# Optimization experiments

Measured on AMD Instinct MI355X. Metric: run time of the kernel, lower is better.

The kernel has to match this reference:

```python
import math
import jax, jax.numpy as jnp
import numpy as np

IN_CH = 64
NUM_ANCHOR = 4
MAP_H, MAP_W = 96, 96
BATCH = 8
BN_EPS = 1e-5


def _conv2d(x, w, b, padding, dilation):
    # x: [B,C,H,W], w: [O,I,kh,kw] (OIHW)
    y = jax.lax.conv_general_dilated(
        x, w, window_strides=(1, 1),
        padding=((padding, padding), (padding, padding)),
        rhs_dilation=(dilation, dilation),
        dimension_numbers=('NCHW', 'OIHW', 'NCHW'))
    return y + b[None, :, None, None]


def _bn(x, gamma, beta, mean, var):
    scale = gamma / jnp.sqrt(var + BN_EPS)
    return x * scale[None, :, None, None] + (beta - mean * scale)[None, :, None, None]


def setup_inputs() -> dict:
    key = jax.random.key(0)
    ks = jax.random.split(key, 12)
    # cyclic channel-shift permutation matrices, one per anchor pass
    eye = np.eye(IN_CH, dtype=np.float32)
    shift = IN_CH // (2 * NUM_ANCHOR)
    perms = np.stack([eye[np.roll(np.arange(IN_CH), i * shift)] for i in range(2 * NUM_ANCHOR)])
    w_std = 1.0 / math.sqrt(IN_CH * 9)
    return {
        'x': jax.random.normal(ks[0], (BATCH, IN_CH, MAP_H, MAP_W), dtype=jnp.float32),
        'perms': jnp.asarray(perms),
        'dcn_w': jax.random.normal(ks[1], (IN_CH, IN_CH, 3, 3), dtype=jnp.float32) * w_std,
        'dcn_b': jax.random.normal(ks[2], (IN_CH,), dtype=jnp.float32) * 0.01,
        'conv2_w': jax.random.normal(ks[3], (IN_CH, IN_CH, 3, 3), dtype=jnp.float32) * w_std,
        'conv2_b': jax.random.normal(ks[4], (IN_CH,), dtype=jnp.float32) * 0.01,
        'conv3_w': jax.random.normal(ks[5], (IN_CH, IN_CH, 3, 3), dtype=jnp.float32) * w_std,
        'conv3_b': jax.random.normal(ks[6], (IN_CH,), dtype=jnp.float32) * 0.01,
        'bn_gamma': jax.random.uniform(ks[7], (3, IN_CH), dtype=jnp.float32, minval=0.5, maxval=1.5),
        'bn_beta': jax.random.normal(ks[8], (3, IN_CH), dtype=jnp.float32) * 0.1,
        'bn_mean': jax.random.normal(ks[9], (3, IN_CH), dtype=jnp.float32) * 0.1,
        'bn_var': jax.random.uniform(ks[10], (3, IN_CH), dtype=jnp.float32, minval=0.5, maxval=1.5),
    }


def reference(x, perms, dcn_w, dcn_b, conv2_w, conv2_b, conv3_w, conv3_b,
              bn_gamma, bn_beta, bn_mean, bn_var):
    h = x.shape[2]
    pad = math.ceil(h / (2 ** 1.5 + 2))  # 20 for h=96

    def conv_stack(o):
        # DCN at init (zero offsets) == plain 3x3 conv, pad=1
        o = jax.nn.relu(_bn(_conv2d(o, dcn_w, dcn_b, 1, 1), bn_gamma[0], bn_beta[0], bn_mean[0], bn_var[0]))
        o = jax.nn.relu(_bn(_conv2d(o, conv2_w, conv2_b, 2, 2), bn_gamma[1], bn_beta[1], bn_mean[1], bn_var[1]))
        o = jax.nn.relu(_bn(_conv2d(o, conv3_w, conv3_b, 2, 2), bn_gamma[2], bn_beta[2], bn_mean[2], bn_var[2]))
        return o

    outs = []
    for i in range(2 * NUM_ANCHOR):  # fixed small structural loop
        o = jnp.einsum('mn,bnhw->bmhw', perms[i], x)  # channel permutation
        if i % 2 != 0:
            o = jnp.pad(o, ((0, 0), (0, 0), (pad, pad), (pad, pad)))
        o = jnp.rot90(o, k=i % 4, axes=(-2, -1))   # ccw rotate
        o = conv_stack(o)
        o = jnp.rot90(o, k=(-i) % 4, axes=(-2, -1))  # cw rotate back
        if i % 2 != 0:
            H, W = o.shape[-2], o.shape[-1]
            sh, sw = (H - MAP_H) // 2, (W - MAP_W) // 2
            o = o[..., sh:sh + MAP_H, sw:sw + MAP_W]  # center crop
        outs.append(o)
    out_tensor = jnp.concatenate(outs, axis=1)  # [B, 8*C, H, W]
    out = jnp.max(out_tensor, axis=1, keepdims=True)
    # branch_name == 'midpoint', orientational_anchor=False -> clamped sigmoid
    return jnp.clip(jax.nn.sigmoid(out), 1e-4, 1.0 - 1e-4)
```

## Files before the change

### kernel.cpp

```cpp
#include <hip/hip_runtime.h>
#include <math.h>

#define B 8
#define C 64
#define HW 96
#define NWV 36864

typedef __attribute__((ext_vector_type(8)))  short short8;
typedef __attribute__((ext_vector_type(16))) float floatx16;

__device__ __forceinline__ unsigned short f2bf(float f) {
    unsigned int u = __float_as_uint(f);
    unsigned int r = (u + 0x7fffu + ((u >> 16) & 1u)) >> 16;
    return (unsigned short)r;
}

__device__ __forceinline__ void rotmap(int k, int ta, int tb, int& sa, int& sb) {
    switch (k) {
        case 0: sa = ta;     sb = tb;     break;
        case 1: sa = 2 - tb; sb = ta;     break;
        case 2: sa = 2 - ta; sb = 2 - tb; break;
        default: sa = tb;    sb = 2 - ta; break;
    }
}

__global__ void prep_w(const float* __restrict__ dcn_w, const float* __restrict__ c2w,
                       const float* __restrict__ c3w,
                       const float* __restrict__ gamma, const float* __restrict__ var_,
                       unsigned short* __restrict__ Wall) {
    int idx = blockIdx.x * 256 + threadIdx.x;
    if (idx >= 16 * NWV) return;
    int v = idx / NWV, rem = idx % NWV;
    int tap  = rem >> 12;
    int w12  = rem & 4095;
    int ks   = w12 >> 10;
    int cf   = (w12 >> 9) & 1;
    int lane = (w12 >> 3) & 63;
    int j    = w12 & 7;
    int co = cf * 32 + (lane & 31);
    int ci = ks * 16 + (lane >> 5) * 8 + j;
    int ta = tap / 3, tb = tap % 3;
    const float* src; int k, srcci, l;
    if (v < 8)       { k = v & 3;  srcci = (ci + 8 * v) & 63; src = dcn_w; l = 0; }
    else if (v < 12) { k = v - 8;  srcci = ci; src = c2w; l = 1; }
    else             { k = v - 12; srcci = ci; src = c3w; l = 2; }
    int sa, sb; rotmap(k, ta, tb, sa, sb);
    float s = gamma[l * 64 + co] * rsqrtf(var_[l * 64 + co] + 1e-5f);
    Wall[idx] = f2bf(src[((co * 64 + srcci) * 3 + sa) * 3 + sb] * s);
}

__global__ void prep_bias(const float* __restrict__ dcn_b, const float* __restrict__ c2b,
                          const float* __restrict__ c3b,
                          const float* __restrict__ gamma, const float* __restrict__ beta,
                          const float* __restrict__ mean, const float* __restrict__ var_,
                          float* __restrict__ biasg) {
    int t = threadIdx.x;
    if (t < 192) {
        int l = t >> 6, c = t & 63;
        const float* cb = (l == 0) ? dcn_b : ((l == 1) ? c2b : c3b);
        float s = gamma[l * 64 + c] * rsqrtf(var_[l * 64 + c] + 1e-5f);
        biasg[t] = cb[c] * s + beta[l * 64 + c] - mean[l * 64 + c] * s;
    }
}

__global__ __launch_bounds__(256) void prep_x(const float* __restrict__ in,
                                              unsigned short* __restrict__ out) {
    __shared__ float row[64 * 97];
    int by = blockIdx.x;
    int b = by / 96, y = by % 96;
    int t = threadIdx.x;
    for (int e = t; e < 6144; e += 256) {
        int c = e / 96, x = e - c * 96;
        row[c * 97 + x] = in[(((size_t)(b * 64 + c) * 96 + y) * 96) + x];
    }
    __syncthreads();
    for (int e = t; e < 6144; e += 256) {
        int x = e >> 6, c = e & 63;
        out[(((size_t)(b * 96 + y) * 96 + x) << 6) + c] = f2bf(row[c * 97 + x]);
    }
}

__global__ __launch_bounds__(256) void border_clear(unsigned short* __restrict__ buf1) {
    int idx = blockIdx.y;
    int br = (idx >> 3) * 2, b = idx & 7;
    int z = br * 8 + b;
    int i = blockIdx.x * 32 + (threadIdx.x >> 3);
    int g = threadIdx.x & 7;
    int r, c;
    if (i < 416)      { r = i / 104;              c = i % 104; }
    else if (i < 832) { int j = i - 416; r = 100 + j / 104; c = j % 104; }
    else              { int j = i - 832; r = 4 + (j >> 3); int c8 = j & 7;
                        c = (c8 < 4) ? c8 : 92 + c8; }
    uint4 zero = make_uint4(0u, 0u, 0u, 0u);
    *(uint4*)(buf1 + (size_t)z * (104 * 104 * 64) + ((size_t)(r * 104 + c) << 6) + (g << 3)) = zero;
}

__global__ __launch_bounds__(256, 2) void conv1_k(
    const unsigned short* __restrict__ xhwc, unsigned short* __restrict__ buf1,
    const unsigned short* __restrict__ Wall, const float* __restrict__ biasg) {

    __shared__ __align__(16) unsigned short xt[10 * 34 * 64];

    int z = blockIdx.z, br = z >> 3, b = z & 7, odd = br & 1;
    int fy0 = blockIdx.y * 8, fx0 = blockIdx.x * 32;
    int t = threadIdx.x, lane = t & 63, wv = t >> 6;
    int n = lane & 31, kq = lane >> 5;

    const unsigned short* xb = xhwc + ((size_t)b * 96 * 96 << 6);
    const short8* Ag = (const short8*)(Wall + (size_t)br * NWV);

    for (int e = t; e < 2720; e += 256) {
        int p = e >> 3, g = e & 7;
        int yy = p / 34, xx = p - yy * 34;
        int gy = fy0 - 5 + yy, gx = fx0 - 5 + xx;
        uint4 v = make_uint4(0u, 0u, 0u, 0u);
        if ((unsigned)gy < 96u && (unsigned)gx < 96u)
            v = *(const uint4*)(xb + ((size_t)(gy * 96 + gx) << 6) + (g << 3));
        *(uint4*)(xt + (p << 6) + ((g ^ (xx & 7)) << 3)) = v;
    }
    __syncthreads();

    floatx16 acc[2][2];
#pragma unroll
    for (int cf = 0; cf < 2; cf++)
#pragma unroll
        for (int pf = 0; pf < 2; pf++)
#pragma unroll
            for (int i = 0; i < 16; i++) acc[cf][pf][i] = 0.f;

#pragma unroll
    for (int ks = 0; ks < 4; ks++) {
#pragma unroll
        for (int tb = 0; tb < 3; tb++) {
            short8 a[3][2];
#pragma unroll
            for (int ta = 0; ta < 3; ta++)
#pragma unroll
                for (int cf = 0; cf < 2; cf++)
                    a[ta][cf] = Ag[(((ta * 3 + tb) * 4 + ks) * 2 + cf) * 64 + lane];
            int xx = n + tb;
            int g = ((ks * 2 + kq) ^ (xx & 7)) << 3;
            short8 bf[4];
#pragma unroll
            for (int rr = 0; rr < 4; rr++) {
                int p = (2 * wv + rr) * 34 + xx;
                bf[rr] = *(const short8*)(xt + (p << 6) + g);
            }
#pragma unroll
            for (int ta = 0; ta < 3; ta++)
#pragma unroll
                for (int pf = 0; pf < 2; pf++) {
                    int rr = pf + ta;
                    acc[0][pf] = __builtin_amdgcn_mfma_f32_32x32x16_bf16(a[ta][0], bf[rr], acc[0][pf], 0, 0, 0);
                    acc[1][pf] = __builtin_amdgcn_mfma_f32_32x32x16_bf16(a[ta][1], bf[rr], acc[1][pf], 0, 0, 0);
                }
        }
    }

    float4 bv[2][4];
#pragma unroll
    for (int cf = 0; cf < 2; cf++)
#pragma unroll
        for (int rb = 0; rb < 4; rb++)
            bv[cf][rb] = *(const float4*)(biasg + 32 * cf + 8 * rb + 4 * kq);

    __syncthreads();
#pragma unroll
    for (int pf = 0; pf < 2; pf++) {
        int pq = (2 * wv + pf) * 32 + n;
        int key = (pq & 7) << 1;
#pragma unroll
        for (int cf = 0; cf < 2; cf++)
#pragma unroll
            for (int rb = 0; rb < 4; rb++) {
                int u = kq + 2 * rb + 8 * cf;
                float v0 = fmaxf(acc[cf][pf][rb * 4 + 0] + bv[cf][rb].x, 0.f);
                float v1 = fmaxf(acc[cf][pf][rb * 4 + 1] + bv[cf][rb].y, 0.f);
                float v2 = fmaxf(acc[cf][pf][rb * 4 + 2] + bv[cf][rb].z, 0.f);
                float v3 = fmaxf(acc[cf][pf][rb * 4 + 3] + bv[cf][rb].w, 0.f);
                uint2 pk = make_uint2((unsigned)f2bf(v0) | ((unsigned)f2bf(v1) << 16),
                                      (unsigned)f2bf(v2) | ((unsigned)f2bf(v3) << 16));
                *(uint2*)((char*)xt + pq * 128 + ((u ^ key) << 3)) = pk;
            }
    }
    __syncthreads();

    unsigned short* fb = buf1 + (size_t)z * (104 * 104 * 64);
    int lo = odd ? 0 : 4, hi = odd ? 104 : 100;
    for (int e = t; e < 2048; e += 256) {
        int px = e >> 3, g = e & 7;
        int key = (px & 7) << 1;
        uint4 v = *(const uint4*)((const char*)xt + px * 128 + (((2 * g) ^ key) << 3));
        int lr = px >> 5, nn = px & 31;
        int f = fy0 + lr, fc = fx0 + nn;
        if (f >= lo && f < hi && fc >= lo && fc < hi)
            *(uint4*)(fb + ((size_t)(f * 104 + fc) << 6) + (g << 3)) = v;
    }
}

__global__ __launch_bounds__(512, 1) void conv23_k(
    const unsigned short* __restrict__ buf1, float* __restrict__ maxb,
    const unsigned short* __restrict__ Wall, const float* __restrict__ biasg) {

    __shared__ __align__(16) unsigned short xs[960 * 20];
    __shared__ __align__(16) unsigned short c2out[720 * 68];

    int z = blockIdx.z, br = z >> 3, odd = br & 1;
    int oy0 = blockIdx.y * 16, ox0 = blockIdx.x * 32;
    int t = threadIdx.x, lane = t & 63, wv = t >> 6;
    int n = lane & 31, kq = lane >> 5;

    const unsigned short* fb = buf1 + (size_t)z * (104 * 104 * 64);
    const short8* A2 = (const short8*)(Wall + (size_t)(8  + (br & 3)) * NWV);
    const short8* A3 = (const short8*)(Wall + (size_t)(12 + (br & 3)) * NWV);

    int q_[3], row2_[3], col2_[3];
#pragma unroll
    for (int jj = 0; jj < 3; jj++) {
        int q = 96 * wv + 32 * jj + n;
        q_[jj] = q;
        int qc = (q < 720) ? q : 719;
        int r2 = qc / 36;
        row2_[jj] = r2;
        col2_[jj] = qc - 36 * r2;
    }

    int sp_off[4], sp_lds[4]; bool sp_on[4];
#pragma unroll
    for (int k2 = 0; k2 < 4; k2++) {
        int e = t + k2 * 512;
        sp_on[k2] = e < 1920;
        int p = e >> 1, g = e & 1;
        if (!sp_on[k2]) { p = 0; g = 0; }
        int yy = p / 40, xx = p - yy * 40;
        sp_off[k2] = (((oy0 + yy) * 104 + ox0 + xx) << 6) + (g << 3);
        sp_lds[k2] = p * 20 + (g << 3);
    }

    uint4 ld[4];
#pragma unroll
    for (int k2 = 0; k2 < 4; k2++)
        if (sp_on[k2]) ld[k2] = *(const uint4*)(fb + sp_off[k2]);

    floatx16 acc2[3][2];
#pragma unroll
    for (int jj = 0; jj < 3; jj++)
#pragma unroll
        for (int cf = 0; cf < 2; cf++)
#pragma unroll
            for (int i = 0; i < 16; i++) acc2[jj][cf][i] = 0.f;

    for (int ks = 0; ks < 4; ks++) {
        if (ks) __syncthreads();
#pragma unroll
        for (int k2 = 0; k2 < 4; k2++)
            if (sp_on[k2]) *(uint4*)(xs + sp_lds[k2]) = ld[k2];
        if (ks < 3) {
#pragma unroll
            for (int k2 = 0; k2 < 4; k2++)
                if (sp_on[k2]) ld[k2] = *(const uint4*)(fb + sp_off[k2] + ((ks + 1) << 4));
        }
        __syncthreads();

#pragma unroll
        for (int tb = 0; tb < 3; tb++) {
            short8 a[3][2];
#pragma unroll
            for (int ta = 0; ta < 3; ta++)
#pragma unroll
                for (int cf = 0; cf < 2; cf++)
                    a[ta][cf] = A2[(((ta * 3 + tb) * 4 + ks) * 2 + cf) * 64 + lane];
            int uoff = kq << 3;
#pragma unroll
            for (int jj = 0; jj < 3; jj++) {
                int colx = col2_[jj] + 2 * tb;
#pragma unroll
                for (int ta = 0; ta < 3; ta++) {
                    int p = (row2_[jj] + 2 * ta) * 40 + colx;
                    short8 bfr = *(const short8*)(xs + p * 20 + uoff);
                    acc2[jj][0] = __builtin_amdgcn_mfma_f32_32x32x16_bf16(a[ta][0], bfr, acc2[jj][0], 0, 0, 0);
                    acc2[jj][1] = __builtin_amdgcn_mfma_f32_32x32x16_bf16(a[ta][1], bfr, acc2[jj][1], 0, 0, 0);
                }
            }
        }
    }

    int rlo2 = (!odd && oy0 == 0)  ? 2  : 0;
    int rhi2 = (!odd && oy0 == 80) ? 18 : 20;
    int clo2 = (!odd && ox0 == 0)  ? 2  : 0;
    int chi2 = (!odd && ox0 == 64) ? 34 : 36;

#pragma unroll
    for (int jj = 0; jj < 3; jj++) {
        if (q_[jj] < 720) {
            bool valid = (row2_[jj] >= rlo2) && (row2_[jj] < rhi2) &&
                         (col2_[jj] >= clo2) && (col2_[jj] < chi2);
#pragma unroll
            for (int cf = 0; cf < 2; cf++)
#pragma unroll
                for (int rb = 0; rb < 4; rb++) {
                    float v0 = 0.f, v1 = 0.f, v2 = 0.f, v3 = 0.f;
                    if (valid) {
                        float4 bb = *(const float4*)(biasg + 64 + 32 * cf + 8 * rb + 4 * kq);
                        v0 = fmaxf(acc2[jj][cf][rb * 4 + 0] + bb.x, 0.f);
                        v1 = fmaxf(acc2[jj][cf][rb * 4 + 1] + bb.y, 0.f);
                        v2 = fmaxf(acc2[jj][cf][rb * 4 + 2] + bb.z, 0.f);
                        v3 = fmaxf(acc2[jj][cf][rb * 4 + 3] + bb.w, 0.f);
                    }
                    uint2 pk = make_uint2((unsigned)f2bf(v0) | ((unsigned)f2bf(v1) << 16),
                                          (unsigned)f2bf(v2) | ((unsigned)f2bf(v3) << 16));
                    *(uint2*)(c2out + q_[jj] * 68 + 32 * cf + 8 * rb + 4 * kq) = pk;
                }
        }
    }
    __syncthreads();

    floatx16 acc3[2][2];
#pragma unroll
    for (int cf = 0; cf < 2; cf++)
#pragma unroll
        for (int pf = 0; pf < 2; pf++)
#pragma unroll
            for (int i = 0; i < 16; i++) acc3[cf][pf][i] = 0.f;

#pragma unroll
    for (int ks = 0; ks < 4; ks++) {
#pragma unroll
        for (int tb = 0; tb < 3; tb++) {
            short8 a[3][2];
#pragma unroll
            for (int ta = 0; ta < 3; ta++)
#pragma unroll
                for (int cf = 0; cf < 2; cf++)
                    a[ta][cf] = A3[(((ta * 3 + tb) * 4 + ks) * 2 + cf) * 64 + lane];
            int col = n + 2 * tb;
            int uoff = (2 * ks + kq) << 3;
            short8 bf[6];
#pragma unroll
            for (int rr = 0; rr < 6; rr++) {
                int q = (2 * wv + rr) * 36 + col;
                bf[rr] = *(const short8*)(c2out + q * 68 + uoff);
            }
#pragma unroll
            for (int ta = 0; ta < 3; ta++)
#pragma unroll
                for (int pf = 0; pf < 2; pf++) {
                    int rr = pf + 2 * ta;
                    acc3[0][pf] = __builtin_amdgcn_mfma_f32_32x32x16_bf16(a[ta][0], bf[rr], acc3[0][pf], 0, 0, 0);
                    acc3[1][pf] = __builtin_amdgcn_mfma_f32_32x32x16_bf16(a[ta][1], bf[rr], acc3[1][pf], 0, 0, 0);
                }
        }
    }

#pragma unroll
    for (int pf = 0; pf < 2; pf++) {
        float m = 0.f;
#pragma unroll
        for (int cf = 0; cf < 2; cf++)
#pragma unroll
            for (int rb = 0; rb < 4; rb++) {
                float4 bb = *(const float4*)(biasg + 128 + 32 * cf + 8 * rb + 4 * kq);
                m = fmaxf(m, acc3[cf][pf][rb * 4 + 0] + bb.x);
                m = fmaxf(m, acc3[cf][pf][rb * 4 + 1] + bb.y);
                m = fmaxf(m, acc3[cf][pf][rb * 4 + 2] + bb.z);
                m = fmaxf(m, acc3[cf][pf][rb * 4 + 3] + bb.w);
            }
        m = fmaxf(m, 0.f);
        m = fmaxf(m, __shfl_xor(m, 32, 64));
        if (lane < 32)
            maxb[((size_t)z * 96 + oy0 + 2 * wv + pf) * 96 + ox0 + n] = m;
    }
}

__global__ void final_k(const float* __restrict__ maxb, float* __restrict__ out) {
    int i = blockIdx.x * 256 + threadIdx.x;
    if (i < B * HW * HW) {
        int b = i / 9216, yx = i - b * 9216;
        float m = 0.f;
#pragma unroll
        for (int br = 0; br < 8; br++)
            m = fmaxf(m, maxb[((size_t)(br * 8 + b)) * 9216 + yx]);
        float v = 1.f / (1.f + expf(-m));
        out[i] = fminf(fmaxf(v, 1e-4f), 1.f - 1e-4f);
    }
}


extern "C" void kernel_launch(void* const* d_in, const int* in_sizes, int n_in,
                              void* d_out, int out_size, void* d_ws, size_t ws_size,
                              hipStream_t stream) {
    const float* x     = (const float*)d_in[0];
    const float* dcn_w = (const float*)d_in[2];
    const float* dcn_b = (const float*)d_in[3];
    const float* c2w   = (const float*)d_in[4];
    const float* c2b   = (const float*)d_in[5];
    const float* c3w   = (const float*)d_in[6];
    const float* c3b   = (const float*)d_in[7];
    const float* gamma = (const float*)d_in[8];
    const float* beta  = (const float*)d_in[9];
    const float* mean  = (const float*)d_in[10];
    const float* var_  = (const float*)d_in[11];

    char* ws = (char*)d_ws;
    unsigned short* Wall = (unsigned short*)ws;
    size_t off = (size_t)16 * NWV * 2;
    float* biasg = (float*)(ws + off);            off += 1024;
    float* maxb  = (float*)(ws + off);            off += (size_t)64 * 9216 * 4;
    unsigned short* xhwc = (unsigned short*)(ws + off); off += (size_t)B * 9216 * 64 * 2;
    unsigned short* buf1 = (unsigned short*)(ws + off);

    prep_w<<<(16 * NWV + 255) / 256, 256, 0, stream>>>(dcn_w, c2w, c3w, gamma, var_, Wall);
    prep_bias<<<1, 256, 0, stream>>>(dcn_b, c2b, c3b, gamma, beta, mean, var_, biasg);
    prep_x<<<B * 96, 256, 0, stream>>>(x, xhwc);
    border_clear<<<dim3(50, 32), 256, 0, stream>>>(buf1);

    dim3 g1(4, 13, 64);
    conv1_k<<<g1, 256, 0, stream>>>(xhwc, buf1, Wall, biasg);

    dim3 g23(3, 6, 64);
    conv23_k<<<g23, 512, 0, stream>>>(buf1, maxb, Wall, biasg);

    final_k<<<(B * HW * HW + 255) / 256, 256, 0, stream>>>(maxb, (float*)d_out);
}
```

Before: 351.1 us.

## Halve conv23 output tile height, re-layout LDS planes, allow two blocks per CU

The fused conv2+conv3 kernel now uses 8-row output tiles instead of 16, which doubles the grid. Its shared-memory buffers move from a padded pixel-major layout to channel-group-major planes. Launch bounds now allow two blocks per CU, and conv3 computes one output row per wave. The aim is more occupancy and latency hiding from the smaller LDS and register footprint. In exchange, the dilated halo is recomputed relative to useful output (12 intermediate rows per 8 outputs versus 20 per 16), which adds conv2 work and more weight loads per output.

```diff
diff --git a/kernel.cpp b/kernel.cpp
--- a/kernel.cpp
+++ b/kernel.cpp
@@ -198,15 +198,15 @@
     }
 }
 
-__global__ __launch_bounds__(512, 1) void conv23_k(
+__global__ __launch_bounds__(512, 2) void conv23_k(
     const unsigned short* __restrict__ buf1, float* __restrict__ maxb,
     const unsigned short* __restrict__ Wall, const float* __restrict__ biasg) {
 
-    __shared__ __align__(16) unsigned short xs[960 * 20];
-    __shared__ __align__(16) unsigned short c2out[720 * 68];
+    __shared__ __align__(16) unsigned short xs[2 * 5120];
+    __shared__ __align__(16) unsigned short c2out[8 * 3456];
 
     int z = blockIdx.z, br = z >> 3, odd = br & 1;
-    int oy0 = blockIdx.y * 16, ox0 = blockIdx.x * 32;
+    int oy0 = blockIdx.y * 8, ox0 = blockIdx.x * 32;
     int t = threadIdx.x, lane = t & 63, wv = t >> 6;
     int n = lane & 31, kq = lane >> 5;
 
@@ -214,37 +214,37 @@
     const short8* A2 = (const short8*)(Wall + (size_t)(8  + (br & 3)) * NWV);
     const short8* A3 = (const short8*)(Wall + (size_t)(12 + (br & 3)) * NWV);
 
-    int q_[3], row2_[3], col2_[3];
-#pragma unroll
-    for (int jj = 0; jj < 3; jj++) {
-        int q = 96 * wv + 32 * jj + n;
+    int q_[2], row2_[2], col2_[2];
+#pragma unroll
+    for (int jj = 0; jj < 2; jj++) {
+        int q = 64 * wv + 32 * jj + n;
         q_[jj] = q;
-        int qc = (q < 720) ? q : 719;
+        int qc = (q < 432) ? q : 431;
         int r2 = qc / 36;
         row2_[jj] = r2;
         col2_[jj] = qc - 36 * r2;
     }
 
-    int sp_off[4], sp_lds[4]; bool sp_on[4];
-#pragma unroll
-    for (int k2 = 0; k2 < 4; k2++) {
+    int sp_off[3], sp_lds[3]; bool sp_on[3];
+#pragma unroll
+    for (int k2 = 0; k2 < 3; k2++) {
         int e = t + k2 * 512;
-        sp_on[k2] = e < 1920;
+        sp_on[k2] = e < 1280;
         int p = e >> 1, g = e & 1;
         if (!sp_on[k2]) { p = 0; g = 0; }
         int yy = p / 40, xx = p - yy * 40;
         sp_off[k2] = (((oy0 + yy) * 104 + ox0 + xx) << 6) + (g << 3);
-        sp_lds[k2] = p * 20 + (g << 3);
-    }
-
-    uint4 ld[4];
-#pragma unroll
-    for (int k2 = 0; k2 < 4; k2++)
+        sp_lds[k2] = g * 5120 + (p << 3);
+    }
+
+    uint4 ld[3];
+#pragma unroll
+    for (int k2 = 0; k2 < 3; k2++)
         if (sp_on[k2]) ld[k2] = *(const uint4*)(fb + sp_off[k2]);
 
-    floatx16 acc2[3][2];
-#pragma unroll
-    for (int jj = 0; jj < 3; jj++)
+    floatx16 acc2[2][2];
+#pragma unroll
+    for (int jj = 0; jj < 2; jj++)
 #pragma unroll
         for (int cf = 0; cf < 2; cf++)
 #pragma unroll
@@ -253,11 +253,11 @@
     for (int ks = 0; ks < 4; ks++) {
         if (ks) __syncthreads();
 #pragma unroll
-        for (int k2 = 0; k2 < 4; k2++)
+        for (int k2 = 0; k2 < 3; k2++)
             if (sp_on[k2]) *(uint4*)(xs + sp_lds[k2]) = ld[k2];
         if (ks < 3) {
 #pragma unroll
-            for (int k2 = 0; k2 < 4; k2++)
+            for (int k2 = 0; k2 < 3; k2++)
                 if (sp_on[k2]) ld[k2] = *(const uint4*)(fb + sp_off[k2] + ((ks + 1) << 4));
         }
         __syncthreads();
@@ -270,14 +270,14 @@
 #pragma unroll
                 for (int cf = 0; cf < 2; cf++)
                     a[ta][cf] = A2[(((ta * 3 + tb) * 4 + ks) * 2 + cf) * 64 + lane];
-            int uoff = kq << 3;
-#pragma unroll
-            for (int jj = 0; jj < 3; jj++) {
+            int uoff = kq * 5120;
+#pragma unroll
+            for (int jj = 0; jj < 2; jj++) {
                 int colx = col2_[jj] + 2 * tb;
 #pragma unroll
                 for (int ta = 0; ta < 3; ta++) {
                     int p = (row2_[jj] + 2 * ta) * 40 + colx;
-                    short8 bfr = *(const short8*)(xs + p * 20 + uoff);
+                    short8 bfr = *(const short8*)(xs + uoff + (p << 3));
                     acc2[jj][0] = __builtin_amdgcn_mfma_f32_32x32x16_bf16(a[ta][0], bfr, acc2[jj][0], 0, 0, 0);
                     acc2[jj][1] = __builtin_amdgcn_mfma_f32_32x32x16_bf16(a[ta][1], bfr, acc2[jj][1], 0, 0, 0);
                 }
@@ -286,13 +286,13 @@
     }
 
     int rlo2 = (!odd && oy0 == 0)  ? 2  : 0;
-    int rhi2 = (!odd && oy0 == 80) ? 18 : 20;
+    int rhi2 = (!odd && oy0 == 88) ? 10 : 12;
     int clo2 = (!odd && ox0 == 0)  ? 2  : 0;
     int chi2 = (!odd && ox0 == 64) ? 34 : 36;
 
 #pragma unroll
-    for (int jj = 0; jj < 3; jj++) {
-        if (q_[jj] < 720) {
+    for (int jj = 0; jj < 2; jj++) {
+        if (q_[jj] < 432) {
             bool valid = (row2_[jj] >= rlo2) && (row2_[jj] < rhi2) &&
                          (col2_[jj] >= clo2) && (col2_[jj] < chi2);
 #pragma unroll
@@ -309,19 +309,17 @@
                     }
                     uint2 pk = make_uint2((unsigned)f2bf(v0) | ((unsigned)f2bf(v1) << 16),
                                           (unsigned)f2bf(v2) | ((unsigned)f2bf(v3) << 16));
-                    *(uint2*)(c2out + q_[jj] * 68 + 32 * cf + 8 * rb + 4 * kq) = pk;
+                    *(uint2*)(c2out + (4 * cf + rb) * 3456 + (q_[jj] << 3) + 4 * kq) = pk;
                 }
         }
     }
     __syncthreads();
 
-    floatx16 acc3[2][2];
+    floatx16 acc3[2];
 #pragma unroll
     for (int cf = 0; cf < 2; cf++)
 #pragma unroll
-        for (int pf = 0; pf < 2; pf++)
-#pragma unroll
-            for (int i = 0; i < 16; i++) acc3[cf][pf][i] = 0.f;
+        for (int i = 0; i < 16; i++) acc3[cf][i] = 0.f;
 
 #pragma unroll
     for (int ks = 0; ks < 4; ks++) {
@@ -334,41 +332,33 @@
                 for (int cf = 0; cf < 2; cf++)
                     a[ta][cf] = A3[(((ta * 3 + tb) * 4 + ks) * 2 + cf) * 64 + lane];
             int col = n + 2 * tb;
-            int uoff = (2 * ks + kq) << 3;
-            short8 bf[6];
-#pragma unroll
-            for (int rr = 0; rr < 6; rr++) {
-                int q = (2 * wv + rr) * 36 + col;
-                bf[rr] = *(const short8*)(c2out + q * 68 + uoff);
+            int uoff = (2 * ks + kq) * 3456;
+#pragma unroll
+            for (int ta = 0; ta < 3; ta++) {
+                int p = (wv + 2 * ta) * 36 + col;
+                short8 bfr = *(const short8*)(c2out + uoff + (p << 3));
+                acc3[0] = __builtin_amdgcn_mfma_f32_32x32x16_bf16(a[ta][0], bfr, acc3[0], 0, 0, 0);
+                acc3[1] = __builtin_amdgcn_mfma_f32_32x32x16_bf16(a[ta][1], bfr, acc3[1], 0, 0, 0);
             }
-#pragma unroll
-            for (int ta = 0; ta < 3; ta++)
-#pragma unroll
-                for (int pf = 0; pf < 2; pf++) {
-                    int rr = pf + 2 * ta;
-                    acc3[0][pf] = __builtin_amdgcn_mfma_f32_32x32x16_bf16(a[ta][0], bf[rr], acc3[0][pf], 0, 0, 0);
-                    acc3[1][pf] = __builtin_amdgcn_mfma_f32_32x32x16_bf16(a[ta][1], bf[rr], acc3[1][pf], 0, 0, 0);
-                }
         }
     }
 
-#pragma unroll
-    for (int pf = 0; pf < 2; pf++) {
+    {
         float m = 0.f;
 #pragma unroll
         for (int cf = 0; cf < 2; cf++)
 #pragma unroll
             for (int rb = 0; rb < 4; rb++) {
                 float4 bb = *(const float4*)(biasg + 128 + 32 * cf + 8 * rb + 4 * kq);
-                m = fmaxf(m, acc3[cf][pf][rb * 4 + 0] + bb.x);
-                m = fmaxf(m, acc3[cf][pf][rb * 4 + 1] + bb.y);
-                m = fmaxf(m, acc3[cf][pf][rb * 4 + 2] + bb.z);
-                m = fmaxf(m, acc3[cf][pf][rb * 4 + 3] + bb.w);
+                m = fmaxf(m, acc3[cf][rb * 4 + 0] + bb.x);
+                m = fmaxf(m, acc3[cf][rb * 4 + 1] + bb.y);
+                m = fmaxf(m, acc3[cf][rb * 4 + 2] + bb.z);
+                m = fmaxf(m, acc3[cf][rb * 4 + 3] + bb.w);
             }
         m = fmaxf(m, 0.f);
         m = fmaxf(m, __shfl_xor(m, 32, 64));
         if (lane < 32)
-            maxb[((size_t)z * 96 + oy0 + 2 * wv + pf) * 96 + ox0 + n] = m;
+            maxb[((size_t)z * 96 + oy0 + wv) * 96 + ox0 + n] = m;
     }
 }
 
@@ -417,7 +407,7 @@
     dim3 g1(4, 13, 64);
     conv1_k<<<g1, 256, 0, stream>>>(xhwc, buf1, Wall, biasg);
 
-    dim3 g23(3, 6, 64);
+    dim3 g23(3, 12, 64);
     conv23_k<<<g23, 512, 0, stream>>>(buf1, maxb, Wall, biasg);
 
     final_k<<<(B * HW * HW + 255) / 256, 256, 0, stream>>>(maxb, (float*)d_out);
```

Result: slower. 378.7 us (+7.8%).
